# Performance work log

Measured on AMD Instinct MI355X. Metric: run time of the kernel, lower is better.

The kernel has to match this reference:

```python
import jax, jax.numpy as jnp
import numpy as np

DELTA = 1e-3  # kernel_delta

B, N, D, K = 256, 131072, 128, 50


def setup_inputs() -> dict:
    key = jax.random.key(0)
    k1, k2, k3 = jax.random.split(key, 3)
    return {
        "key": jax.random.normal(k1, (B, D), dtype=jnp.float32),
        "keys": jax.random.normal(k2, (N, D), dtype=jnp.float32),
        "values": jax.random.normal(k3, (N, 1), dtype=jnp.float32),
        "num_neighbours": K,
    }


def reference(key, keys, values, num_neighbours):
    # Squared L2 distance via GEMM expansion (same math as
    # torch.square(torch.norm(key[:,None]-keys, dim=-1)))
    q_sq = jnp.sum(key * key, axis=1, keepdims=True)          # [B,1]
    d_sq = jnp.sum(keys * keys, axis=1)                        # [N]
    cross = key @ keys.T                                       # [B,N] GEMM
    dist2 = jnp.maximum(q_sq + d_sq[None, :] - 2.0 * cross, 0.0)
    # inverse-distance-weighting kernel
    weights = 1.0 / (dist2 + DELTA)                            # [B,N]
    # top-k mask + renormalize (non-topk weights are zeroed, so the
    # normalized sum reduces to a sum over the top-k entries)
    top_w, top_idx = jax.lax.top_k(weights, num_neighbours)    # [B,K]
    w_norm = top_w / jnp.sum(top_w, axis=1, keepdims=True)     # [B,K]
    # gather matched values and weighted sum
    v = values[top_idx, 0]                                     # [B,K]
    output = jnp.sum(w_norm * v, axis=1, keepdims=True)        # [B,1]
    return output
```

## Files before the change

kernel.cpp:

```cpp
#include <hip/hip_runtime.h>

#define BQ 256
#define NK 131072
#define DIM 128
#define KT2 128
#define NCH2 (NK / KT2)
#define SAMP 8192
#define SBLK (SAMP / KT2)
#define CPB_MAIN 4
#define GRID_MAIN (NCH2 / CPB_MAIN)
#define CAPB 16
#define CAPL 8192
#define NB2 4096
#define DELTA 1e-3f

typedef __attribute__((ext_vector_type(8))) short bf16x8;
typedef __attribute__((ext_vector_type(4))) float f32x4;

__device__ __forceinline__ unsigned short f2bf(float x) {
    unsigned u = __float_as_uint(x);
    u += 0x7fffu + ((u >> 16) & 1u);
    return (unsigned short)(u >> 16);
}
__device__ __forceinline__ float bf2f(unsigned short h) {
    return __uint_as_float(((unsigned)h) << 16);
}
__device__ __forceinline__ int kclamp(int K) {
    if (K < 1) K = 1;
    if (K > 256) K = 256;
    return K;
}
__device__ __forceinline__ void cvt8(const float4 a, const float4 b,
                                     bf16x8& hv, bf16x8& lv, float& sq) {
    float xs[8] = { a.x, a.y, a.z, a.w, b.x, b.y, b.z, b.w };
    sq = 0.f;
    #pragma unroll
    for (int i = 0; i < 8; ++i) {
        unsigned short h = f2bf(xs[i]);
        hv[i] = (short)h;
        lv[i] = (short)f2bf(xs[i] - bf2f(h));
        sq = fmaf(xs[i], xs[i], sq);
    }
}

__global__ __launch_bounds__(256, 4)
void p0_prep(const float* __restrict__ qkey,
             unsigned short* __restrict__ qhG, unsigned short* __restrict__ qlG,
             float* __restrict__ qsqg)
{
    const int item = blockIdx.x * 256 + threadIdx.x;
    const int r = item >> 4, d0 = (item & 15) * 8;
    const float* src = qkey + (r << 7) + d0;
    float4 a = *(const float4*)src, b = *(const float4*)(src + 4);
    bf16x8 hv, lv; float s;
    cvt8(a, b, hv, lv, s);
    *(bf16x8*)(qhG + (r << 7) + d0) = hv;
    *(bf16x8*)(qlG + (r << 7) + d0) = lv;
    #pragma unroll
    for (int off = 1; off < 16; off <<= 1) s += __shfl_xor(s, off, 16);
    if ((threadIdx.x & 15) == 0) qsqg[r] = s;
}

template<bool FILTER>
__global__ __launch_bounds__(1024, 4)
void kmfma(const unsigned short* __restrict__ qhG, const unsigned short* __restrict__ qlG,
           const float* __restrict__ keys, const float* __restrict__ qsqg,
           const float* __restrict__ values, float* __restrict__ dout,
           const unsigned* __restrict__ tau, int* __restrict__ cntmat,
           uint2* __restrict__ cand, int cpb)
{
    __shared__ __align__(16) unsigned short khs[KT2 * DIM];
    __shared__ __align__(16) unsigned short kls[KT2 * DIM];
    __shared__ float    ksq_s[KT2];
    __shared__ float    qsq_s[BQ];
    __shared__ unsigned tau_s[BQ];
    __shared__ int      lcnt[2][BQ];

    const int tid  = threadIdx.x;
    const int lane = tid & 63, wv = tid >> 6;
    const int fr = lane & 15, fg = lane >> 4;

    if (tid < BQ) {
        qsq_s[tid] = qsqg[tid];
        if (FILTER) { tau_s[tid] = tau[tid]; lcnt[0][tid] = 0; lcnt[1][tid] = 0; }
    }

    bf16x8 qh[4], ql[4];
    #pragma unroll
    for (int s = 0; s < 4; ++s) {
        int off = ((wv * 16 + fr) << 7) + s * 32 + fg * 8;
        qh[s] = *(const bf16x8*)(qhG + off);
        ql[s] = *(const bf16x8*)(qlG + off);
    }

    const int r0 = tid >> 4;
    const int d0 = (tid & 15) * 8;

    float4 ra0, rb0, ra1, rb1;
    int ch = blockIdx.x * cpb;
    {
        const float* s0 = keys + (size_t)ch * (KT2 * DIM) + tid * 8;
        ra0 = *(const float4*)s0;          rb0 = *(const float4*)(s0 + 4);
        ra1 = *(const float4*)(s0 + 8192); rb1 = *(const float4*)(s0 + 8192 + 4);
    }

    for (int c = 0; c < cpb; ++c, ++ch) {
        {
            bf16x8 hv, lv; float sq;
            cvt8(ra0, rb0, hv, lv, sq);
            unsigned byte = ((unsigned)((r0 << 8) + (d0 << 1))) ^ (unsigned)((r0 & 7) << 4);
            *(bf16x8*)((char*)khs + byte) = hv;
            *(bf16x8*)((char*)kls + byte) = lv;
            #pragma unroll
            for (int off = 1; off < 16; off <<= 1) sq += __shfl_xor(sq, off, 16);
            if ((tid & 15) == 0) ksq_s[r0] = sq;
            const int r1 = r0 + 64;
            cvt8(ra1, rb1, hv, lv, sq);
            byte = ((unsigned)((r1 << 8) + (d0 << 1))) ^ (unsigned)((r1 & 7) << 4);
            *(bf16x8*)((char*)khs + byte) = hv;
            *(bf16x8*)((char*)kls + byte) = lv;
            #pragma unroll
            for (int off = 1; off < 16; off <<= 1) sq += __shfl_xor(sq, off, 16);
            if ((tid & 15) == 0) ksq_s[r1] = sq;
        }
        __syncthreads();

        if (c + 1 < cpb) {
            const float* s0 = keys + (size_t)(ch + 1) * (KT2 * DIM) + tid * 8;
            ra0 = *(const float4*)s0;          rb0 = *(const float4*)(s0 + 4);
            ra1 = *(const float4*)(s0 + 8192); rb1 = *(const float4*)(s0 + 8192 + 4);
        }

        f32x4 acc[8];
        #pragma unroll
        for (int kf = 0; kf < 8; ++kf) acc[kf] = f32x4{0.f, 0.f, 0.f, 0.f};

        #pragma unroll
        for (int s = 0; s < 4; ++s) {
            #pragma unroll
            for (int kf = 0; kf < 8; ++kf) {
                const int krow = kf * 16 + fr;
                const int dd   = s * 32 + fg * 8;
                unsigned byte = ((unsigned)((krow << 8) + (dd << 1))) ^ (unsigned)((krow & 7) << 4);
                bf16x8 bh = *(bf16x8*)((char*)khs + byte);
                bf16x8 bl = *(bf16x8*)((char*)kls + byte);
                acc[kf] = __builtin_amdgcn_mfma_f32_16x16x32_bf16(qh[s], bh, acc[kf], 0, 0, 0);
                acc[kf] = __builtin_amdgcn_mfma_f32_16x16x32_bf16(ql[s], bh, acc[kf], 0, 0, 0);
                acc[kf] = __builtin_amdgcn_mfma_f32_16x16x32_bf16(qh[s], bl, acc[kf], 0, 0, 0);
            }
        }

        float qsqv[4];
        #pragma unroll
        for (int rg = 0; rg < 4; ++rg) qsqv[rg] = qsq_s[wv * 16 + fg * 4 + rg];
        #pragma unroll
        for (int kf = 0; kf < 8; ++kf) {
            const int kcol = kf * 16 + fr;
            const int k = ch * KT2 + kcol;
            const float kq = ksq_s[kcol];
            f32x4 a = acc[kf];
            #pragma unroll
            for (int rg = 0; rg < 4; ++rg) {
                const int q = wv * 16 + fg * 4 + rg;
                float dv = fmaxf(qsqv[rg] + kq - 2.f * a[rg], 0.f);
                if (FILTER) {
                    if (dv <= __uint_as_float(tau_s[q])) {
                        int slot = atomicAdd(&lcnt[c & 1][q], 1);
                        if (slot < CAPB)
                            cand[((size_t)q * NCH2 + ch) * CAPB + slot] =
                                make_uint2(__float_as_uint(dv), __float_as_uint(values[k]));
                    }
                } else {
                    dout[(size_t)q * SAMP + k] = dv;
                }
            }
        }
        __syncthreads();
        if (FILTER && tid < BQ) {
            int cc2 = lcnt[c & 1][tid]; if (cc2 > CAPB) cc2 = CAPB;
            lcnt[c & 1][tid] = 0;
            cntmat[(size_t)tid * NCH2 + ch] = cc2;
        }
    }
}

__global__ __launch_bounds__(256, 4)
void k2_tau(const float* __restrict__ dsamp, const int* __restrict__ pK,
            unsigned* __restrict__ tau)
{
    const int q = blockIdx.x, tid = threadIdx.x;
    const int lane = tid & 63, wid = tid >> 6;
    const int K = kclamp(*pK);

    unsigned eb[32];
    const float4* row4 = (const float4*)(dsamp + (size_t)q * SAMP);
    #pragma unroll
    for (int i = 0; i < 8; ++i) {
        float4 v = row4[tid + 256 * i];
        eb[4*i+0] = __float_as_uint(v.x); eb[4*i+1] = __float_as_uint(v.y);
        eb[4*i+2] = __float_as_uint(v.z); eb[4*i+3] = __float_as_uint(v.w);
    }

    __shared__ int red[4];
    __shared__ unsigned go;
    unsigned lo = 0u, hi = 0x7f7fffffu;
    while (lo < hi) {
        unsigned mid = lo + ((hi - lo) >> 1);
        int c = 0;
        #pragma unroll
        for (int i = 0; i < 32; ++i) c += (eb[i] <= mid) ? 1 : 0;
        #pragma unroll
        for (int off = 32; off; off >>= 1) c += __shfl_down(c, off, 64);
        if (lane == 0) red[wid] = c;
        __syncthreads();
        if (tid == 0) go = ((red[0] + red[1] + red[2] + red[3]) >= K) ? 1u : 0u;
        __syncthreads();
        if (go) hi = mid; else lo = mid + 1;
        __syncthreads();
    }
    if (tid == 0) tau[q] = lo;
}

__global__ __launch_bounds__(256)
void k4_final(const uint2* __restrict__ cand, const int* __restrict__ cntmat,
              const unsigned* __restrict__ tau, const int* __restrict__ pK,
              float* __restrict__ out)
{
    const int q = blockIdx.x, tid = threadIdx.x;
    const int lane = tid & 63, wid = tid >> 6;
    const int K = kclamp(*pK);

    __shared__ uint2    list[CAPL];
    __shared__ int      hist2[NB2];
    __shared__ unsigned bcand[256];
    __shared__ int      wtot[4];
    __shared__ int      red[4];
    __shared__ unsigned go;
    __shared__ int      s_bb, s_cb, s_m;
    __shared__ unsigned s_T;
    __shared__ unsigned long long s_S;

    int4 c4 = ((const int4*)(cntmat + (size_t)q * NCH2))[tid];
    int mysum = c4.x + c4.y + c4.z + c4.w;
    int incl = mysum;
    #pragma unroll
    for (int off = 1; off < 64; off <<= 1) {
        int t = __shfl_up(incl, off, 64);
        if (lane >= off) incl += t;
    }
    if (lane == 63) wtot[wid] = incl;
    for (int i = tid; i < NB2; i += 256) hist2[i] = 0;
    if (tid == 0) {
        s_m = 0; s_bb = NB2; s_cb = 0;
        s_S = (((unsigned long long)NB2) << 32) / ((unsigned long long)tau[q] + 1ULL);
    }
    __syncthreads();
    int base = incl - mysum;
    #pragma unroll
    for (int w = 0; w < 4; ++w) if (w < wid) base += wtot[w];
    const int total = wtot[0] + wtot[1] + wtot[2] + wtot[3];

    {
        int off = base;
        const uint2* seg = cand + ((size_t)q * NCH2 + tid * 4) * CAPB;
        int cc[4] = { c4.x, c4.y, c4.z, c4.w };
        #pragma unroll
        for (int s2 = 0; s2 < 4; ++s2) {
            #pragma unroll 1
            for (int j = 0; j < cc[s2]; ++j) {
                if (off < CAPL) list[off] = seg[s2 * CAPB + j];
                ++off;
            }
        }
    }
    __syncthreads();
    const int n = (total > CAPL) ? CAPL : total;
    const unsigned long long S = s_S;

    for (int i = tid; i < n; i += 256)
        atomicAdd(&hist2[(unsigned)(((unsigned long long)list[i].x * S) >> 32)], 1);
    __syncthreads();

    int h[16], sum16 = 0;
    #pragma unroll
    for (int b = 0; b < 16; ++b) { h[b] = hist2[tid * 16 + b]; sum16 += h[b]; }
    int incl2 = sum16;
    #pragma unroll
    for (int off = 1; off < 64; off <<= 1) {
        int t = __shfl_up(incl2, off, 64);
        if (lane >= off) incl2 += t;
    }
    if (lane == 63) red[wid] = incl2;
    __syncthreads();
    int base2 = incl2 - sum16;
    #pragma unroll
    for (int w = 0; w < 4; ++w) if (w < wid) base2 += red[w];
    if (base2 < K) {
        int c = base2;
        #pragma unroll
        for (int b = 0; b < 16; ++b) {
            if (c < K && c + h[b] >= K) { s_bb = tid * 16 + b; s_cb = c; }
            c += h[b];
        }
    }
    __syncthreads();
    const int bb = s_bb, cbelow = s_cb, R2 = K - cbelow;

    for (int i = tid; i < n; i += 256) {
        unsigned bits = list[i].x;
        if ((int)(unsigned)(((unsigned long long)bits * S) >> 32) == bb) {
            int sl = atomicAdd(&s_m, 1);
            if (sl < 256) bcand[sl] = bits;
        }
    }
    __syncthreads();
    const int m = s_m;
    if (m <= 256) {
        if (tid < m) {
            unsigned bi = bcand[tid];
            int cl = 0, ceq = 0;
            for (int j = 0; j < m; ++j) {
                unsigned bj = bcand[j];
                cl += (bj < bi) ? 1 : 0; ceq += (bj == bi) ? 1 : 0;
            }
            if (cl < R2 && R2 <= cl + ceq) s_T = bi;
        }
    } else {
        unsigned lo = 0u, hi = tau[q];
        while (lo < hi) {
            unsigned mid = lo + ((hi - lo) >> 1);
            int c = 0;
            for (int i = tid; i < n; i += 256) c += (list[i].x <= mid) ? 1 : 0;
            #pragma unroll
            for (int off = 32; off; off >>= 1) c += __shfl_down(c, off, 64);
            if (lane == 0) red[wid] = c;
            __syncthreads();
            if (tid == 0) go = ((red[0] + red[1] + red[2] + red[3]) >= K) ? 1u : 0u;
            __syncthreads();
            if (go) hi = mid; else lo = mid + 1;
            __syncthreads();
        }
        if (tid == 0) s_T = lo;
    }
    __syncthreads();
    const unsigned T = s_T;

    double sw = 0.0, swv = 0.0, sevt = 0.0;
    int cl = 0, ce = 0;
    for (int i = tid; i < n; i += 256) {
        unsigned b = list[i].x;
        float d = __uint_as_float(b), v = __uint_as_float(list[i].y);
        if (b < T) {
            double w = 1.0 / ((double)d + (double)DELTA);
            cl += 1; sw += w; swv += w * (double)v;
        } else if (b == T) { ce += 1; sevt += (double)v; }
    }
    #pragma unroll
    for (int off = 32; off; off >>= 1) {
        sw   += __shfl_down(sw,   off, 64);
        swv  += __shfl_down(swv,  off, 64);
        sevt += __shfl_down(sevt, off, 64);
        cl   += __shfl_down(cl,   off, 64);
        ce   += __shfl_down(ce,   off, 64);
    }
    __shared__ double dred[3][4];
    __shared__ int    ired[2][4];
    if (lane == 0) { dred[0][wid] = sw; dred[1][wid] = swv; dred[2][wid] = sevt;
                     ired[0][wid] = cl; ired[1][wid] = ce; }
    __syncthreads();
    if (tid == 0) {
        double SW = 0, SWV = 0, SEVT = 0; int CL = 0, CE = 0;
        #pragma unroll
        for (int w = 0; w < 4; ++w) { SW += dred[0][w]; SWV += dred[1][w]; SEVT += dred[2][w];
                                      CL += ired[0][w]; CE += ired[1][w]; }
        double wT = 1.0 / ((double)__uint_as_float(T) + (double)DELTA);
        double need = (double)(K - CL);
        double num = SWV + wT * (need / (double)CE) * SEVT;
        double den = SW + wT * need;
        out[q] = (float)(num / den);
    }
}

extern "C" void kernel_launch(void* const* d_in, const int* in_sizes, int n_in,
                              void* d_out, int out_size, void* d_ws, size_t ws_size,
                              hipStream_t stream)
{
    const float* qkey   = (const float*)d_in[0];
    const float* keys   = (const float*)d_in[1];
    const float* values = (const float*)d_in[2];
    const int*   pK     = (const int*)d_in[3];
    float* out = (float*)d_out;

    char* w = (char*)d_ws;
    float*          qsqg  = (float*)w;
    unsigned short* qhG   = (unsigned short*)(w + 4096);
    unsigned short* qlG   = (unsigned short*)(w + 4096 + 65536);
    float*          dsamp = (float*)(w + 135168);
    unsigned*       tauB  = (unsigned*)(w + 8523776);
    int*            cntmat= (int*)(w + 8527872);
    uint2*          cand  = (uint2*)(w + 9576448);

    p0_prep<<<dim3(16), dim3(256), 0, stream>>>(qkey, qhG, qlG, qsqg);
    kmfma<false><<<dim3(SBLK), dim3(1024), 0, stream>>>(qhG, qlG, keys, qsqg, values,
                                                        dsamp, tauB, cntmat, cand, 1);
    k2_tau<<<dim3(BQ), dim3(256), 0, stream>>>(dsamp, pK, tauB);
    kmfma<true><<<dim3(GRID_MAIN), dim3(1024), 0, stream>>>(qhG, qlG, keys, qsqg, values,
                                                            dsamp, tauB, cntmat, cand, CPB_MAIN);
    k4_final<<<dim3(BQ), dim3(256), 0, stream>>>(cand, cntmat, tauB, pK, out);
}
```

Measured before the change: 128.5 us.

## Split query batch across two 512-thread blocks per key chunk group

The MFMA distance kernel now launches twice as many 512-thread blocks, each covering half of the 256 queries for a given range of key chunks. Each thread loads four key rows instead of two. Values for the current chunk are now staged in shared memory instead of being gathered from global memory per candidate. The count matrix is transposed to chunk-major so the split blocks write it coalesced, and the final kernel reads it strided. The cost is that each key chunk is loaded and converted to bf16 twice, in exchange for more blocks to spread across compute units and fewer registers per block.

```diff
diff --git a/kernel.cpp b/kernel.cpp
--- a/kernel.cpp
+++ b/kernel.cpp
@@ -8,7 +8,8 @@
 #define SAMP 8192
 #define SBLK (SAMP / KT2)
 #define CPB_MAIN 4
-#define GRID_MAIN (NCH2 / CPB_MAIN)
+#define GRID_MAIN ((NCH2 / CPB_MAIN) * 2)
+#define QH 128
 #define CAPB 16
 #define CAPL 8192
 #define NB2 4096
@@ -62,7 +63,7 @@
 }
 
 template<bool FILTER>
-__global__ __launch_bounds__(1024, 4)
+__global__ __launch_bounds__(512, 4)
 void kmfma(const unsigned short* __restrict__ qhG, const unsigned short* __restrict__ qlG,
            const float* __restrict__ keys, const float* __restrict__ qsqg,
            const float* __restrict__ values, float* __restrict__ dout,
@@ -72,23 +73,26 @@
     __shared__ __align__(16) unsigned short khs[KT2 * DIM];
     __shared__ __align__(16) unsigned short kls[KT2 * DIM];
     __shared__ float    ksq_s[KT2];
-    __shared__ float    qsq_s[BQ];
-    __shared__ unsigned tau_s[BQ];
-    __shared__ int      lcnt[2][BQ];
+    __shared__ float    qsq_s[QH];
+    __shared__ float    vals_s[KT2];
+    __shared__ unsigned tau_s[QH];
+    __shared__ int      lcnt[2][QH];
 
     const int tid  = threadIdx.x;
     const int lane = tid & 63, wv = tid >> 6;
     const int fr = lane & 15, fg = lane >> 4;
-
-    if (tid < BQ) {
-        qsq_s[tid] = qsqg[tid];
-        if (FILTER) { tau_s[tid] = tau[tid]; lcnt[0][tid] = 0; lcnt[1][tid] = 0; }
+    const int qoff = (blockIdx.x & 1) * QH;
+    const int cg   = blockIdx.x >> 1;
+
+    if (tid < QH) {
+        qsq_s[tid] = qsqg[qoff + tid];
+        if (FILTER) { tau_s[tid] = tau[qoff + tid]; lcnt[0][tid] = 0; lcnt[1][tid] = 0; }
     }
 
     bf16x8 qh[4], ql[4];
     #pragma unroll
     for (int s = 0; s < 4; ++s) {
-        int off = ((wv * 16 + fr) << 7) + s * 32 + fg * 8;
+        int off = ((qoff + wv * 16 + fr) << 7) + s * 32 + fg * 8;
         qh[s] = *(const bf16x8*)(qhG + off);
         ql[s] = *(const bf16x8*)(qlG + off);
     }
@@ -96,39 +100,60 @@
     const int r0 = tid >> 4;
     const int d0 = (tid & 15) * 8;
 
-    float4 ra0, rb0, ra1, rb1;
-    int ch = blockIdx.x * cpb;
+    float4 ra0, rb0, ra1, rb1, ra2, rb2, ra3, rb3;
+    float  vpre;
+    int ch = cg * cpb;
     {
         const float* s0 = keys + (size_t)ch * (KT2 * DIM) + tid * 8;
-        ra0 = *(const float4*)s0;          rb0 = *(const float4*)(s0 + 4);
-        ra1 = *(const float4*)(s0 + 8192); rb1 = *(const float4*)(s0 + 8192 + 4);
+        ra0 = *(const float4*)s0;            rb0 = *(const float4*)(s0 + 4);
+        ra1 = *(const float4*)(s0 + 4096);   rb1 = *(const float4*)(s0 + 4096 + 4);
+        ra2 = *(const float4*)(s0 + 8192);   rb2 = *(const float4*)(s0 + 8192 + 4);
+        ra3 = *(const float4*)(s0 + 12288);  rb3 = *(const float4*)(s0 + 12288 + 4);
+        vpre = (tid < KT2) ? values[ch * KT2 + tid] : 0.f;
     }
 
     for (int c = 0; c < cpb; ++c, ++ch) {
         {
-            bf16x8 hv, lv; float sq;
+            bf16x8 hv, lv; float sq; unsigned byte; int rr;
+            rr = r0;
             cvt8(ra0, rb0, hv, lv, sq);
-            unsigned byte = ((unsigned)((r0 << 8) + (d0 << 1))) ^ (unsigned)((r0 & 7) << 4);
-            *(bf16x8*)((char*)khs + byte) = hv;
-            *(bf16x8*)((char*)kls + byte) = lv;
+            byte = ((unsigned)((rr << 8) + (d0 << 1))) ^ (unsigned)((rr & 7) << 4);
+            *(bf16x8*)((char*)khs + byte) = hv;  *(bf16x8*)((char*)kls + byte) = lv;
             #pragma unroll
             for (int off = 1; off < 16; off <<= 1) sq += __shfl_xor(sq, off, 16);
-            if ((tid & 15) == 0) ksq_s[r0] = sq;
-            const int r1 = r0 + 64;
+            if ((tid & 15) == 0) ksq_s[rr] = sq;
+            rr = r0 + 32;
             cvt8(ra1, rb1, hv, lv, sq);
-            byte = ((unsigned)((r1 << 8) + (d0 << 1))) ^ (unsigned)((r1 & 7) << 4);
-            *(bf16x8*)((char*)khs + byte) = hv;
-            *(bf16x8*)((char*)kls + byte) = lv;
+            byte = ((unsigned)((rr << 8) + (d0 << 1))) ^ (unsigned)((rr & 7) << 4);
+            *(bf16x8*)((char*)khs + byte) = hv;  *(bf16x8*)((char*)kls + byte) = lv;
             #pragma unroll
             for (int off = 1; off < 16; off <<= 1) sq += __shfl_xor(sq, off, 16);
-            if ((tid & 15) == 0) ksq_s[r1] = sq;
-        }
+            if ((tid & 15) == 0) ksq_s[rr] = sq;
+            rr = r0 + 64;
+            cvt8(ra2, rb2, hv, lv, sq);
+            byte = ((unsigned)((rr << 8) + (d0 << 1))) ^ (unsigned)((rr & 7) << 4);
+            *(bf16x8*)((char*)khs + byte) = hv;  *(bf16x8*)((char*)kls + byte) = lv;
+            #pragma unroll
+            for (int off = 1; off < 16; off <<= 1) sq += __shfl_xor(sq, off, 16);
+            if ((tid & 15) == 0) ksq_s[rr] = sq;
+            rr = r0 + 96;
+            cvt8(ra3, rb3, hv, lv, sq);
+            byte = ((unsigned)((rr << 8) + (d0 << 1))) ^ (unsigned)((rr & 7) << 4);
+            *(bf16x8*)((char*)khs + byte) = hv;  *(bf16x8*)((char*)kls + byte) = lv;
+            #pragma unroll
+            for (int off = 1; off < 16; off <<= 1) sq += __shfl_xor(sq, off, 16);
+            if ((tid & 15) == 0) ksq_s[rr] = sq;
+        }
+        if (tid < KT2) vals_s[tid] = vpre;
         __syncthreads();
 
         if (c + 1 < cpb) {
             const float* s0 = keys + (size_t)(ch + 1) * (KT2 * DIM) + tid * 8;
-            ra0 = *(const float4*)s0;          rb0 = *(const float4*)(s0 + 4);
-            ra1 = *(const float4*)(s0 + 8192); rb1 = *(const float4*)(s0 + 8192 + 4);
+            ra0 = *(const float4*)s0;            rb0 = *(const float4*)(s0 + 4);
+            ra1 = *(const float4*)(s0 + 4096);   rb1 = *(const float4*)(s0 + 4096 + 4);
+            ra2 = *(const float4*)(s0 + 8192);   rb2 = *(const float4*)(s0 + 8192 + 4);
+            ra3 = *(const float4*)(s0 + 12288);  rb3 = *(const float4*)(s0 + 12288 + 4);
+            vpre = (tid < KT2) ? values[(ch + 1) * KT2 + tid] : 0.f;
         }
 
         f32x4 acc[8];
@@ -161,25 +186,25 @@
             f32x4 a = acc[kf];
             #pragma unroll
             for (int rg = 0; rg < 4; ++rg) {
-                const int q = wv * 16 + fg * 4 + rg;
+                const int qloc = wv * 16 + fg * 4 + rg;
                 float dv = fmaxf(qsqv[rg] + kq - 2.f * a[rg], 0.f);
                 if (FILTER) {
-                    if (dv <= __uint_as_float(tau_s[q])) {
-                        int slot = atomicAdd(&lcnt[c & 1][q], 1);
+                    if (dv <= __uint_as_float(tau_s[qloc])) {
+                        int slot = atomicAdd(&lcnt[c & 1][qloc], 1);
                         if (slot < CAPB)
-                            cand[((size_t)q * NCH2 + ch) * CAPB + slot] =
-                                make_uint2(__float_as_uint(dv), __float_as_uint(values[k]));
+                            cand[((size_t)(qoff + qloc) * NCH2 + ch) * CAPB + slot] =
+                                make_uint2(__float_as_uint(dv), __float_as_uint(vals_s[kcol]));
                     }
                 } else {
-                    dout[(size_t)q * SAMP + k] = dv;
+                    dout[(size_t)(qoff + qloc) * SAMP + k] = dv;
                 }
             }
         }
         __syncthreads();
-        if (FILTER && tid < BQ) {
+        if (FILTER && tid < QH) {
             int cc2 = lcnt[c & 1][tid]; if (cc2 > CAPB) cc2 = CAPB;
             lcnt[c & 1][tid] = 0;
-            cntmat[(size_t)tid * NCH2 + ch] = cc2;
+            cntmat[(size_t)ch * BQ + qoff + tid] = cc2;
         }
     }
 }
@@ -240,8 +265,12 @@
     __shared__ unsigned s_T;
     __shared__ unsigned long long s_S;
 
-    int4 c4 = ((const int4*)(cntmat + (size_t)q * NCH2))[tid];
-    int mysum = c4.x + c4.y + c4.z + c4.w;
+    int cc[4]; int mysum = 0;
+    #pragma unroll
+    for (int j = 0; j < 4; ++j) {
+        cc[j] = cntmat[(size_t)(tid * 4 + j) * BQ + q];
+        mysum += cc[j];
+    }
     int incl = mysum;
     #pragma unroll
     for (int off = 1; off < 64; off <<= 1) {
@@ -262,13 +291,12 @@
 
     {
         int off = base;
-        const uint2* seg = cand + ((size_t)q * NCH2 + tid * 4) * CAPB;
-        int cc[4] = { c4.x, c4.y, c4.z, c4.w };
         #pragma unroll
         for (int s2 = 0; s2 < 4; ++s2) {
+            const uint2* seg = cand + ((size_t)q * (NK / KT2) + (tid * 4 + s2)) * CAPB;
             #pragma unroll 1
             for (int j = 0; j < cc[s2]; ++j) {
-                if (off < CAPL) list[off] = seg[s2 * CAPB + j];
+                if (off < CAPL) list[off] = seg[j];
                 ++off;
             }
         }
@@ -401,10 +429,10 @@
     uint2*          cand  = (uint2*)(w + 9576448);
 
     p0_prep<<<dim3(16), dim3(256), 0, stream>>>(qkey, qhG, qlG, qsqg);
-    kmfma<false><<<dim3(SBLK), dim3(1024), 0, stream>>>(qhG, qlG, keys, qsqg, values,
-                                                        dsamp, tauB, cntmat, cand, 1);
+    kmfma<false><<<dim3(SBLK * 2), dim3(512), 0, stream>>>(qhG, qlG, keys, qsqg, values,
+                                                           dsamp, tauB, cntmat, cand, 1);
     k2_tau<<<dim3(BQ), dim3(256), 0, stream>>>(dsamp, pK, tauB);
-    kmfma<true><<<dim3(GRID_MAIN), dim3(1024), 0, stream>>>(qhG, qlG, keys, qsqg, values,
-                                                            dsamp, tauB, cntmat, cand, CPB_MAIN);
+    kmfma<true><<<dim3(GRID_MAIN), dim3(512), 0, stream>>>(qhG, qlG, keys, qsqg, values,
+                                                           dsamp, tauB, cntmat, cand, CPB_MAIN);
     k4_final<<<dim3(BQ), dim3(256), 0, stream>>>(cand, cntmat, tauB, pK, out);
 }
```

New measurement: 146.2 us. 1.14x slower.

## Precompute bf16 key planes and stream them into LDS via async global_load_lds

Applied to the files above, without the earlier changes.

Adds a separate prep kernel that converts all keys into swizzled bf16 hi/lo planes plus per-key squared norms once. The MFMA kernels then double-buffer those planes into LDS with direct global-to-LDS loads instead of converting fp32 keys in registers per chunk. The wave tiling changes to 2 query fragments by 4 key fragments for more B-fragment reuse, and cntmat is transposed for coalesced writes. In exchange this adds an extra pass writing and reading about 64MB of planes, more traffic than the original 64MB fp32 read, and 128KB LDS per block, which limits occupancy.

```diff
diff --git a/kernel.cpp b/kernel.cpp
--- a/kernel.cpp
+++ b/kernel.cpp
@@ -6,13 +6,14 @@
 #define KT2 128
 #define NCH2 (NK / KT2)
 #define SAMP 8192
-#define SBLK (SAMP / KT2)
+#define SCH (SAMP / KT2)
 #define CPB_MAIN 4
 #define GRID_MAIN (NCH2 / CPB_MAIN)
 #define CAPB 16
 #define CAPL 8192
 #define NB2 4096
 #define DELTA 1e-3f
+#define CHB 65536
 
 typedef __attribute__((ext_vector_type(8))) short bf16x8;
 typedef __attribute__((ext_vector_type(4))) float f32x4;
@@ -41,6 +42,11 @@
         lv[i] = (short)f2bf(xs[i] - bf2f(h));
         sq = fmaf(xs[i], xs[i], sq);
     }
+}
+__device__ __forceinline__ void gload16(const void* g, void* l) {
+    __builtin_amdgcn_global_load_lds(
+        (const __attribute__((address_space(1))) unsigned int*)g,
+        (__attribute__((address_space(3))) unsigned int*)l, 16, 0, 0);
 }
 
 __global__ __launch_bounds__(256, 4)
@@ -61,125 +67,137 @@
     if ((threadIdx.x & 15) == 0) qsqg[r] = s;
 }
 
+__global__ __launch_bounds__(256, 4)
+void p0k_prep(const float* __restrict__ keys,
+              unsigned char* __restrict__ planes, float* __restrict__ ksqg)
+{
+    const int ch = blockIdx.x;
+    const int t = threadIdx.x;
+    unsigned char* pl = planes + (size_t)ch * CHB;
+    const float* kc = keys + (size_t)ch * (KT2 * DIM);
+    #pragma unroll
+    for (int p = 0; p < 8; ++p) {
+        int flat = p * 2048 + t * 8;
+        int rr = flat >> 7, d0 = flat & 127;
+        const float* src = kc + flat;
+        float4 a = *(const float4*)src, b = *(const float4*)(src + 4);
+        bf16x8 hv, lv; float sq;
+        cvt8(a, b, hv, lv, sq);
+        unsigned byte = (unsigned)(rr * 256 + ((d0 * 2) ^ ((rr & 7) << 4)));
+        *(bf16x8*)(pl + byte) = hv;
+        *(bf16x8*)(pl + 32768 + byte) = lv;
+        #pragma unroll
+        for (int off = 1; off < 16; off <<= 1) sq += __shfl_xor(sq, off, 16);
+        if ((t & 15) == 0) ksqg[ch * KT2 + rr] = sq;
+    }
+}
+
 template<bool FILTER>
 __global__ __launch_bounds__(1024, 4)
-void kmfma(const unsigned short* __restrict__ qhG, const unsigned short* __restrict__ qlG,
-           const float* __restrict__ keys, const float* __restrict__ qsqg,
-           const float* __restrict__ values, float* __restrict__ dout,
-           const unsigned* __restrict__ tau, int* __restrict__ cntmat,
-           uint2* __restrict__ cand, int cpb)
-{
-    __shared__ __align__(16) unsigned short khs[KT2 * DIM];
-    __shared__ __align__(16) unsigned short kls[KT2 * DIM];
-    __shared__ float    ksq_s[KT2];
+void k3_mfma(const unsigned short* __restrict__ qhG, const unsigned short* __restrict__ qlG,
+             const unsigned char* __restrict__ planes, const float* __restrict__ qsqg,
+             const float* __restrict__ ksqg, const float* __restrict__ values,
+             float* __restrict__ dout, const unsigned* __restrict__ tau,
+             int* __restrict__ cntmat, uint2* __restrict__ cand, int cpb)
+{
+    __shared__ __align__(16) unsigned char kbuf[2][CHB];
     __shared__ float    qsq_s[BQ];
     __shared__ unsigned tau_s[BQ];
     __shared__ int      lcnt[2][BQ];
 
-    const int tid  = threadIdx.x;
+    const int tid = threadIdx.x;
     const int lane = tid & 63, wv = tid >> 6;
     const int fr = lane & 15, fg = lane >> 4;
+    const int qg = wv >> 1, ks = wv & 1;
 
     if (tid < BQ) {
         qsq_s[tid] = qsqg[tid];
         if (FILTER) { tau_s[tid] = tau[tid]; lcnt[0][tid] = 0; lcnt[1][tid] = 0; }
     }
 
-    bf16x8 qh[4], ql[4];
-    #pragma unroll
-    for (int s = 0; s < 4; ++s) {
-        int off = ((wv * 16 + fr) << 7) + s * 32 + fg * 8;
-        qh[s] = *(const bf16x8*)(qhG + off);
-        ql[s] = *(const bf16x8*)(qlG + off);
-    }
-
-    const int r0 = tid >> 4;
-    const int d0 = (tid & 15) * 8;
-
-    float4 ra0, rb0, ra1, rb1;
+    bf16x8 qh[2][4], ql[2][4];
+    #pragma unroll
+    for (int qf = 0; qf < 2; ++qf)
+        #pragma unroll
+        for (int s = 0; s < 4; ++s) {
+            int off = ((qg * 32 + qf * 16 + fr) << 7) + s * 32 + fg * 8;
+            qh[qf][s] = *(const bf16x8*)(qhG + off);
+            ql[qf][s] = *(const bf16x8*)(qlG + off);
+        }
+
     int ch = blockIdx.x * cpb;
     {
-        const float* s0 = keys + (size_t)ch * (KT2 * DIM) + tid * 8;
-        ra0 = *(const float4*)s0;          rb0 = *(const float4*)(s0 + 4);
-        ra1 = *(const float4*)(s0 + 8192); rb1 = *(const float4*)(s0 + 8192 + 4);
-    }
+        const unsigned char* g = planes + (size_t)ch * CHB + wv * 4096 + lane * 16;
+        unsigned char* l = &kbuf[0][wv * 4096];
+        gload16(g, l);                 gload16(g + 1024, l + 1024);
+        gload16(g + 2048, l + 2048);   gload16(g + 3072, l + 3072);
+    }
+    __syncthreads();
 
     for (int c = 0; c < cpb; ++c, ++ch) {
-        {
-            bf16x8 hv, lv; float sq;
-            cvt8(ra0, rb0, hv, lv, sq);
-            unsigned byte = ((unsigned)((r0 << 8) + (d0 << 1))) ^ (unsigned)((r0 & 7) << 4);
-            *(bf16x8*)((char*)khs + byte) = hv;
-            *(bf16x8*)((char*)kls + byte) = lv;
+        const int par = c & 1;
+        if (c + 1 < cpb) {
+            const unsigned char* g = planes + (size_t)(ch + 1) * CHB + wv * 4096 + lane * 16;
+            unsigned char* l = &kbuf[par ^ 1][wv * 4096];
+            gload16(g, l);                 gload16(g + 1024, l + 1024);
+            gload16(g + 2048, l + 2048);   gload16(g + 3072, l + 3072);
+        }
+
+        const unsigned char* buf = &kbuf[par][0];
+        f32x4 acc[2][4];
+        #pragma unroll
+        for (int qf = 0; qf < 2; ++qf)
             #pragma unroll
-            for (int off = 1; off < 16; off <<= 1) sq += __shfl_xor(sq, off, 16);
-            if ((tid & 15) == 0) ksq_s[r0] = sq;
-            const int r1 = r0 + 64;
-            cvt8(ra1, rb1, hv, lv, sq);
-            byte = ((unsigned)((r1 << 8) + (d0 << 1))) ^ (unsigned)((r1 & 7) << 4);
-            *(bf16x8*)((char*)khs + byte) = hv;
-            *(bf16x8*)((char*)kls + byte) = lv;
-            #pragma unroll
-            for (int off = 1; off < 16; off <<= 1) sq += __shfl_xor(sq, off, 16);
-            if ((tid & 15) == 0) ksq_s[r1] = sq;
-        }
-        __syncthreads();
-
-        if (c + 1 < cpb) {
-            const float* s0 = keys + (size_t)(ch + 1) * (KT2 * DIM) + tid * 8;
-            ra0 = *(const float4*)s0;          rb0 = *(const float4*)(s0 + 4);
-            ra1 = *(const float4*)(s0 + 8192); rb1 = *(const float4*)(s0 + 8192 + 4);
-        }
-
-        f32x4 acc[8];
-        #pragma unroll
-        for (int kf = 0; kf < 8; ++kf) acc[kf] = f32x4{0.f, 0.f, 0.f, 0.f};
+            for (int kf = 0; kf < 4; ++kf) acc[qf][kf] = f32x4{0.f, 0.f, 0.f, 0.f};
 
         #pragma unroll
         for (int s = 0; s < 4; ++s) {
             #pragma unroll
-            for (int kf = 0; kf < 8; ++kf) {
-                const int krow = kf * 16 + fr;
-                const int dd   = s * 32 + fg * 8;
-                unsigned byte = ((unsigned)((krow << 8) + (dd << 1))) ^ (unsigned)((krow & 7) << 4);
-                bf16x8 bh = *(bf16x8*)((char*)khs + byte);
-                bf16x8 bl = *(bf16x8*)((char*)kls + byte);
-                acc[kf] = __builtin_amdgcn_mfma_f32_16x16x32_bf16(qh[s], bh, acc[kf], 0, 0, 0);
-                acc[kf] = __builtin_amdgcn_mfma_f32_16x16x32_bf16(ql[s], bh, acc[kf], 0, 0, 0);
-                acc[kf] = __builtin_amdgcn_mfma_f32_16x16x32_bf16(qh[s], bl, acc[kf], 0, 0, 0);
-            }
-        }
-
-        float qsqv[4];
-        #pragma unroll
-        for (int rg = 0; rg < 4; ++rg) qsqv[rg] = qsq_s[wv * 16 + fg * 4 + rg];
-        #pragma unroll
-        for (int kf = 0; kf < 8; ++kf) {
-            const int kcol = kf * 16 + fr;
-            const int k = ch * KT2 + kcol;
-            const float kq = ksq_s[kcol];
-            f32x4 a = acc[kf];
-            #pragma unroll
-            for (int rg = 0; rg < 4; ++rg) {
-                const int q = wv * 16 + fg * 4 + rg;
-                float dv = fmaxf(qsqv[rg] + kq - 2.f * a[rg], 0.f);
-                if (FILTER) {
-                    if (dv <= __uint_as_float(tau_s[q])) {
-                        int slot = atomicAdd(&lcnt[c & 1][q], 1);
-                        if (slot < CAPB)
-                            cand[((size_t)q * NCH2 + ch) * CAPB + slot] =
-                                make_uint2(__float_as_uint(dv), __float_as_uint(values[k]));
-                    }
-                } else {
-                    dout[(size_t)q * SAMP + k] = dv;
+            for (int kf = 0; kf < 4; ++kf) {
+                const int krow = ks * 64 + kf * 16 + fr;
+                const unsigned byte =
+                    (unsigned)(krow * 256 + ((s * 64 + fg * 16) ^ ((krow & 7) << 4)));
+                bf16x8 bh = *(const bf16x8*)(buf + byte);
+                bf16x8 bl = *(const bf16x8*)(buf + 32768 + byte);
+                #pragma unroll
+                for (int qf = 0; qf < 2; ++qf) {
+                    acc[qf][kf] = __builtin_amdgcn_mfma_f32_16x16x32_bf16(qh[qf][s], bh, acc[qf][kf], 0, 0, 0);
+                    acc[qf][kf] = __builtin_amdgcn_mfma_f32_16x16x32_bf16(ql[qf][s], bh, acc[qf][kf], 0, 0, 0);
+                    acc[qf][kf] = __builtin_amdgcn_mfma_f32_16x16x32_bf16(qh[qf][s], bl, acc[qf][kf], 0, 0, 0);
                 }
             }
         }
+
+        #pragma unroll
+        for (int kf = 0; kf < 4; ++kf) {
+            const int kcol = ks * 64 + kf * 16 + fr;
+            const int k = ch * KT2 + kcol;
+            const float kq = ksqg[k];
+            #pragma unroll
+            for (int qf = 0; qf < 2; ++qf) {
+                f32x4 a = acc[qf][kf];
+                #pragma unroll
+                for (int rg = 0; rg < 4; ++rg) {
+                    const int q = qg * 32 + qf * 16 + fg * 4 + rg;
+                    float dv = fmaxf(qsq_s[q] + kq - 2.f * a[rg], 0.f);
+                    if (FILTER) {
+                        if (dv <= __uint_as_float(tau_s[q])) {
+                            int slot = atomicAdd(&lcnt[par][q], 1);
+                            if (slot < CAPB)
+                                cand[((size_t)q * NCH2 + ch) * CAPB + slot] =
+                                    make_uint2(__float_as_uint(dv), __float_as_uint(values[k]));
+                        }
+                    } else {
+                        dout[(size_t)q * SAMP + k] = dv;
+                    }
+                }
+            }
+        }
         __syncthreads();
         if (FILTER && tid < BQ) {
-            int cc2 = lcnt[c & 1][tid]; if (cc2 > CAPB) cc2 = CAPB;
-            lcnt[c & 1][tid] = 0;
-            cntmat[(size_t)tid * NCH2 + ch] = cc2;
+            int cc2 = lcnt[par][tid]; if (cc2 > CAPB) cc2 = CAPB;
+            lcnt[par][tid] = 0;
+            cntmat[(size_t)ch * BQ + tid] = cc2;
         }
     }
 }
@@ -240,8 +258,12 @@
     __shared__ unsigned s_T;
     __shared__ unsigned long long s_S;
 
-    int4 c4 = ((const int4*)(cntmat + (size_t)q * NCH2))[tid];
-    int mysum = c4.x + c4.y + c4.z + c4.w;
+    int cc[4]; int mysum = 0;
+    #pragma unroll
+    for (int j = 0; j < 4; ++j) {
+        cc[j] = cntmat[(size_t)(tid * 4 + j) * BQ + q];
+        mysum += cc[j];
+    }
     int incl = mysum;
     #pragma unroll
     for (int off = 1; off < 64; off <<= 1) {
@@ -262,13 +284,12 @@
 
     {
         int off = base;
-        const uint2* seg = cand + ((size_t)q * NCH2 + tid * 4) * CAPB;
-        int cc[4] = { c4.x, c4.y, c4.z, c4.w };
         #pragma unroll
         for (int s2 = 0; s2 < 4; ++s2) {
+            const uint2* seg = cand + ((size_t)q * NCH2 + (tid * 4 + s2)) * CAPB;
             #pragma unroll 1
             for (int j = 0; j < cc[s2]; ++j) {
-                if (off < CAPL) list[off] = seg[s2 * CAPB + j];
+                if (off < CAPL) list[off] = seg[j];
                 ++off;
             }
         }
@@ -304,7 +325,7 @@
         }
     }
     __syncthreads();
-    const int bb = s_bb, cbelow = s_cb, R2 = K - cbelow;
+    const int bb = s_bb, R2 = K - s_cb;
 
     for (int i = tid; i < n; i += 256) {
         unsigned bits = list[i].x;
@@ -399,12 +420,15 @@
     unsigned*       tauB  = (unsigned*)(w + 8523776);
     int*            cntmat= (int*)(w + 8527872);
     uint2*          cand  = (uint2*)(w + 9576448);
+    float*          ksqg  = (float*)(w + 43130880);
+    unsigned char*  planes= (unsigned char*)(w + 43655168);
 
     p0_prep<<<dim3(16), dim3(256), 0, stream>>>(qkey, qhG, qlG, qsqg);
-    kmfma<false><<<dim3(SBLK), dim3(1024), 0, stream>>>(qhG, qlG, keys, qsqg, values,
-                                                        dsamp, tauB, cntmat, cand, 1);
+    p0k_prep<<<dim3(NCH2), dim3(256), 0, stream>>>(keys, planes, ksqg);
+    k3_mfma<false><<<dim3(SCH), dim3(1024), 0, stream>>>(qhG, qlG, planes, qsqg, ksqg, values,
+                                                         dsamp, tauB, cntmat, cand, 1);
     k2_tau<<<dim3(BQ), dim3(256), 0, stream>>>(dsamp, pK, tauB);
-    kmfma<true><<<dim3(GRID_MAIN), dim3(1024), 0, stream>>>(qhG, qlG, keys, qsqg, values,
-                                                            dsamp, tauB, cntmat, cand, CPB_MAIN);
+    k3_mfma<true><<<dim3(GRID_MAIN), dim3(1024), 0, stream>>>(qhG, qlG, planes, qsqg, ksqg, values,
+                                                              dsamp, tauB, cntmat, cand, CPB_MAIN);
     k4_final<<<dim3(BQ), dim3(256), 0, stream>>>(cand, cntmat, tauB, pK, out);
 }
```

After: 130.4 us. Within noise of the previous version (+1.5%).
